# Kernel tuning notes

Hardware: AMD Instinct MI355X
Metric: run time of the kernel (lower is better)

The kernel has to match this reference:

```python
import jax, jax.numpy as jnp
import numpy as np

DIM = 2      # qudit dimension
N = 24       # number of qudits -> D = 2**24 amplitudes
C = 0        # control qudit (index[0])
T = 1        # target qudit (index[1])
J = 1        # j level (code uses j-1)
K = 2        # k level (code uses k-1)
D = DIM ** N
B = 2        # batch of statevectors


def setup_inputs() -> dict:
    key = jax.random.key(0)
    k1, k2, k3 = jax.random.split(key, 3)
    x_real = jax.random.normal(k1, (D, B), dtype=jnp.float32)
    x_imag = jax.random.normal(k2, (D, B), dtype=jnp.float32)
    angle = np.pi * jax.random.normal(k3, (1,), dtype=jnp.float32)
    return {"x_real": x_real, "x_imag": x_imag, "angle": angle}


def reference(x_real, x_imag, angle):
    # Faithful CRY: for each control digit g, rotate target levels (J-1, K-1)
    # by angle g*theta/2 with block [[cos, -sin], [-sin, cos]] (both off-diag
    # entries are -sin, exactly as in the torch source), identity elsewhere.
    psi = (x_real + 1j * x_imag).astype(jnp.complex64)  # (D, B)
    theta = angle[0]
    g = jnp.arange(DIM, dtype=jnp.float32)              # control digit values
    ang = g * theta / 2
    cosv = jnp.cos(ang).astype(jnp.complex64)
    sinv = jnp.sin(ang).astype(jnp.complex64)
    jm, km = J - 1, K - 1
    # M[g, a, b]: per-control-level target-space matrix (DIM x DIM)
    M = jnp.broadcast_to(jnp.eye(DIM, dtype=jnp.complex64), (DIM, DIM, DIM))
    M = M.at[:, jm, jm].set(cosv)
    M = M.at[:, km, km].set(cosv)
    M = M.at[:, jm, km].set(-sinv)
    M = M.at[:, km, jm].set(-sinv)
    pre = DIM ** C
    mid = DIM ** (T - C - 1)
    suf = DIM ** (N - 1 - T)
    # big-endian digit layout: (pre, control, mid, target, suffix, batch)
    psi6 = psi.reshape(pre, DIM, mid, DIM, suf, B)
    out = jnp.einsum('gab,pgmbsB->pgmasB', M, psi6).reshape(D, B)
    # return real/imag stacked as float32 (complex not in harness dtype set)
    return jnp.stack([out.real, out.imag]).astype(jnp.float32)
```

## Files before the change

### kernel.cpp

```cpp
#include <hip/hip_runtime.h>


typedef float v4f __attribute__((ext_vector_type(4)));

__global__ __launch_bounds__(256) void cry_kernel(
    const float* __restrict__ xr_, const float* __restrict__ xi_,
    const float* __restrict__ ang_, float* __restrict__ out_)
{
    const unsigned tid = blockIdx.x * 256u + threadIdx.x;

    float sv, cv;
    __sincosf(0.5f * ang_[0], &sv, &cv);

    const v4f* xr  = (const v4f*)xr_;
    const v4f* xi  = (const v4f*)xi_;
    v4f*       out = (v4f*)out_;

    const unsigned Q  = 1u << 21;
    const unsigned CS = 1u << 22;
    const unsigned IM = 1u << 23;

    v4f cr0 = __builtin_nontemporal_load(xr + tid);
    v4f cr1 = __builtin_nontemporal_load(xr + tid + Q);
    v4f ci0 = __builtin_nontemporal_load(xi + tid);
    v4f ci1 = __builtin_nontemporal_load(xi + tid + Q);
    v4f ar  = __builtin_nontemporal_load(xr + CS + tid);
    v4f br  = __builtin_nontemporal_load(xr + CS + tid + Q);
    v4f ai  = __builtin_nontemporal_load(xi + CS + tid);
    v4f bi  = __builtin_nontemporal_load(xi + CS + tid + Q);

    v4f rr0 = cv * ar - sv * br;
    v4f rr1 = cv * br - sv * ar;
    v4f ri0 = cv * ai - sv * bi;
    v4f ri1 = cv * bi - sv * ai;

    __builtin_nontemporal_store(cr0, out + tid);
    __builtin_nontemporal_store(cr1, out + tid + Q);
    __builtin_nontemporal_store(ci0, out + IM + tid);
    __builtin_nontemporal_store(ci1, out + IM + tid + Q);
    __builtin_nontemporal_store(rr0, out + CS + tid);
    __builtin_nontemporal_store(rr1, out + CS + tid + Q);
    __builtin_nontemporal_store(ri0, out + IM + CS + tid);
    __builtin_nontemporal_store(ri1, out + IM + CS + tid + Q);
}

extern "C" void kernel_launch(void* const* d_in, const int* in_sizes, int n_in,
                              void* d_out, int out_size, void* d_ws, size_t ws_size,
                              hipStream_t stream) {
    const float* xr  = (const float*)d_in[0];
    const float* xi  = (const float*)d_in[1];
    const float* ang = (const float*)d_in[2];
    float* out = (float*)d_out;

    const int threads = 256;
    const int blocks  = (1u << 21) / threads;
    cry_kernel<<<blocks, threads, 0, stream>>>(xr, xi, ang, out);
}
```

Before: 434.8 us.

## Split work into separate copy blocks and rotation blocks with finer granularity

```diff
diff --git a/kernel.cpp b/kernel.cpp
--- a/kernel.cpp
+++ b/kernel.cpp
@@ -7,10 +7,8 @@
     const float* __restrict__ xr_, const float* __restrict__ xi_,
     const float* __restrict__ ang_, float* __restrict__ out_)
 {
-    const unsigned tid = blockIdx.x * 256u + threadIdx.x;
-
-    float sv, cv;
-    __sincosf(0.5f * ang_[0], &sv, &cv);
+    const unsigned bid  = blockIdx.x;
+    const unsigned lane = threadIdx.x;
 
     const v4f* xr  = (const v4f*)xr_;
     const v4f* xi  = (const v4f*)xi_;
@@ -20,28 +18,30 @@
     const unsigned CS = 1u << 22;
     const unsigned IM = 1u << 23;
 
-    v4f cr0 = __builtin_nontemporal_load(xr + tid);
-    v4f cr1 = __builtin_nontemporal_load(xr + tid + Q);
-    v4f ci0 = __builtin_nontemporal_load(xi + tid);
-    v4f ci1 = __builtin_nontemporal_load(xi + tid + Q);
-    v4f ar  = __builtin_nontemporal_load(xr + CS + tid);
-    v4f br  = __builtin_nontemporal_load(xr + CS + tid + Q);
-    v4f ai  = __builtin_nontemporal_load(xi + CS + tid);
-    v4f bi  = __builtin_nontemporal_load(xi + CS + tid + Q);
+    if (bid < 32768u) {
+        const unsigned plane = bid >> 14;
+        const unsigned off   = (bid & 16383u) * 256u + lane;
+        const v4f* src = plane ? xi : xr;
+        v4f v = __builtin_nontemporal_load(src + off);
+        __builtin_nontemporal_store(v, out + plane * IM + off);
+    } else {
+        float sv, cv;
+        __sincosf(0.5f * ang_[0], &sv, &cv);
+        const unsigned rb    = bid - 32768u;
+        const unsigned plane = rb >> 13;
+        const unsigned off   = (rb & 8191u) * 256u + lane;
+        const v4f* src = plane ? xi : xr;
 
-    v4f rr0 = cv * ar - sv * br;
-    v4f rr1 = cv * br - sv * ar;
-    v4f ri0 = cv * ai - sv * bi;
-    v4f ri1 = cv * bi - sv * ai;
+        v4f a = __builtin_nontemporal_load(src + CS + off);
+        v4f b = __builtin_nontemporal_load(src + CS + off + Q);
 
-    __builtin_nontemporal_store(cr0, out + tid);
-    __builtin_nontemporal_store(cr1, out + tid + Q);
-    __builtin_nontemporal_store(ci0, out + IM + tid);
-    __builtin_nontemporal_store(ci1, out + IM + tid + Q);
-    __builtin_nontemporal_store(rr0, out + CS + tid);
-    __builtin_nontemporal_store(rr1, out + CS + tid + Q);
-    __builtin_nontemporal_store(ri0, out + IM + CS + tid);
-    __builtin_nontemporal_store(ri1, out + IM + CS + tid + Q);
+        v4f r0 = cv * a - sv * b;
+        v4f r1 = cv * b - sv * a;
+
+        v4f* dst = out + plane * IM + CS + off;
+        __builtin_nontemporal_store(r0, dst);
+        __builtin_nontemporal_store(r1, dst + Q);
+    }
 }
 
 extern "C" void kernel_launch(void* const* d_in, const int* in_sizes, int n_in,
@@ -53,6 +53,6 @@
     float* out = (float*)d_out;
 
     const int threads = 256;
-    const int blocks  = (1u << 21) / threads;
+    const int blocks  = 32768 + 16384;
     cry_kernel<<<blocks, threads, 0, stream>>>(xr, xi, ang, out);
 }
```

Result: faster. 419.0 us (-3.6%).
